# Kernel tuning notes

Hardware: AMD Instinct MI355X
Metric: run time of the kernel (lower is better)

## Reference

```python
import jax, jax.numpy as jnp
import numpy as np

B, L, D, H, DH, DL, NB = 8, 1024, 512, 8, 64, 64, 128
EPS = 1e-6


def layer_norm(x, g, b):
    m = jnp.mean(x, axis=-1, keepdims=True)
    v = jnp.mean((x - m) ** 2, axis=-1, keepdims=True)
    return (x - m) * jax.lax.rsqrt(v + EPS) * g + b


def rel_bias(timestamps, pos_w, ts_w):
    # position part: skew trick, pos_w has length 2L-1
    t = jnp.concatenate([pos_w, jnp.zeros((L,), pos_w.dtype)])  # (3L-1,)
    t = jnp.tile(t, L)[:-L].reshape(L, 3 * L - 2)
    rel_pos = t[:, L - 1:2 * L - 1]  # (L, L)
    # timestamp part: bucketized pairwise diffs of extended timestamps
    ext = jnp.concatenate([timestamps, timestamps[:, L - 1:L]], axis=1)  # (B, L+1)
    d = ext[:, 1:, None] - ext[:, None, :-1]  # (B, L, L)
    mag = jnp.maximum(jnp.abs(d).astype(jnp.float32), 1.0)
    bucket = jnp.clip((jnp.log(mag) / 0.301).astype(jnp.int32), 0, NB)
    rel_ts = ts_w[bucket]  # (B, L, L)
    return rel_pos[None] + rel_ts


def setup_inputs() -> dict:
    key = jax.random.key(0)
    ks = jax.random.split(key, 8)
    x = jax.random.normal(ks[0], (B, L, D), dtype=jnp.float32)
    timestamps = jnp.sort(jax.random.randint(ks[1], (B, L), 0, 1000000, dtype=jnp.int64), axis=1)
    attn_mask = jnp.triu(jnp.ones((L, L), jnp.float32), k=1)[None, None]  # 1 = masked (future)
    total_out = 2 * DL * H + 2 * DH * H
    uvqk_w = jax.random.normal(ks[2], (D, total_out), dtype=jnp.float32) * 0.02
    out_w = jax.random.normal(ks[3], (DL * H, D), dtype=jnp.float32) * 0.02
    out_b = jnp.zeros((D,), jnp.float32)
    ln1_g = jnp.ones((D,), jnp.float32); ln1_b = jnp.zeros((D,), jnp.float32)
    ln2_g = jnp.ones((DL * H,), jnp.float32); ln2_b = jnp.zeros((DL * H,), jnp.float32)
    ts_weights = jax.random.normal(ks[4], (NB + 1,), dtype=jnp.float32) * 0.02
    pos_weights = jax.random.normal(ks[5], (2 * L - 1,), dtype=jnp.float32) * 0.02
    return {"x": x, "timestamps": timestamps, "attn_mask": attn_mask,
            "uvqk_w": uvqk_w, "out_w": out_w, "out_b": out_b,
            "ln1_g": ln1_g, "ln1_b": ln1_b, "ln2_g": ln2_g, "ln2_b": ln2_b,
            "ts_weights": ts_weights, "pos_weights": pos_weights}


def reference(x, timestamps, attn_mask, uvqk_w, out_w, out_b,
              ln1_g, ln1_b, ln2_g, ln2_b, ts_weights, pos_weights):
    z = layer_norm(x, ln1_g, ln1_b)
    z = jax.nn.silu(z @ uvqk_w)  # linear_activation == 'silu'
    u, v, q, k = jnp.split(z, [DL * H, 2 * DL * H, 2 * DL * H + DH * H], axis=-1)
    q = q.reshape(B, L, H, DH)
    k = k.reshape(B, L, H, DH)
    v = v.reshape(B, L, H, DL)
    scores = jnp.einsum('bmhd,bnhd->bhmn', q, k)
    scores = scores + rel_bias(timestamps, pos_weights, ts_weights)[:, None]
    scores = jax.nn.silu(scores) / L * (1.0 - attn_mask)
    z = jnp.einsum('bhmn,bnhd->bmhd', scores, v).reshape(B, L, H * DL)
    z = layer_norm(z, ln2_g, ln2_b) * u  # gated LN
    return z @ out_w + out_b + x
```

## Files before the change

### kernel.cpp

```cpp
#include <hip/hip_runtime.h>
#include <math.h>

constexpr int Bc = 8;
constexpr int Lc = 1024;
constexpr int Dc = 512;
constexpr int Hc = 8;
constexpr int DHc = 64;
constexpr int DLc = 64;
constexpr int NBc = 128;
constexpr int TOTAL_OUT = 2 * DLc * Hc + 2 * DHc * Hc;
constexpr int ROWS = Bc * Lc;

using f32x4 = __attribute__((ext_vector_type(4))) float;
using s16x8 = __attribute__((ext_vector_type(8))) short;

__device__ __forceinline__ float bf2f(ushort u) {
    union { unsigned int i; float f; } v; v.i = ((unsigned int)u) << 16; return v.f;
}
__device__ __forceinline__ ushort f2bf(float f) {
    union { float f; unsigned int i; } v; v.f = f;
    unsigned int r = v.i + 0x7fffu + ((v.i >> 16) & 1u);
    return (ushort)(r >> 16);
}
__device__ __forceinline__ float silu(float x) {
    float e = __expf(-x);
    return x * __builtin_amdgcn_rcpf(1.0f + e);
}

__global__ __launch_bounds__(256) void transpose_cast(const float* __restrict__ in,
                                                      ushort* __restrict__ out,
                                                      int R, int C) {
    __shared__ float tile[32][33];
    int bc = blockIdx.x * 32, br = blockIdx.y * 32;
    int tx = threadIdx.x & 31, ty = threadIdx.x >> 5;
    for (int i = ty; i < 32; i += 8) {
        int r = br + i, c = bc + tx;
        tile[i][tx] = (r < R && c < C) ? in[(size_t)r * C + c] : 0.f;
    }
    __syncthreads();
    for (int i = ty; i < 32; i += 8) {
        int c = bc + i, r = br + tx;
        if (c < C && r < R) out[(size_t)c * R + r] = f2bf(tile[tx][i]);
    }
}

__global__ __launch_bounds__(256) void ln1_kernel(const float* __restrict__ x,
                                                  const float* __restrict__ g,
                                                  const float* __restrict__ bta,
                                                  ushort* __restrict__ outp) {
    int wid = threadIdx.x >> 6, lane = threadIdx.x & 63;
    int row = blockIdx.x * 4 + wid;
    const float4* xr = (const float4*)(x + (size_t)row * Dc);
    float4 a = xr[lane * 2], c = xr[lane * 2 + 1];
    float xv[8] = {a.x, a.y, a.z, a.w, c.x, c.y, c.z, c.w};
    float s = 0.f, q = 0.f;
#pragma unroll
    for (int i = 0; i < 8; i++) { s += xv[i]; q += xv[i] * xv[i]; }
#pragma unroll
    for (int off = 32; off; off >>= 1) { s += __shfl_xor(s, off); q += __shfl_xor(q, off); }
    float mean = s * (1.f / 512.f);
    float var  = q * (1.f / 512.f) - mean * mean;
    float rstd = rsqrtf(var + 1e-6f);
    const float4* gv = (const float4*)g; const float4* bv = (const float4*)bta;
    float4 g0 = gv[lane * 2], g1 = gv[lane * 2 + 1];
    float4 b0 = bv[lane * 2], b1 = bv[lane * 2 + 1];
    float G[8] = {g0.x, g0.y, g0.z, g0.w, g1.x, g1.y, g1.z, g1.w};
    float Bv[8] = {b0.x, b0.y, b0.z, b0.w, b1.x, b1.y, b1.z, b1.w};
    union { ushort u16[8]; uint4 v; } pk;
#pragma unroll
    for (int i = 0; i < 8; i++) pk.u16[i] = f2bf((xv[i] - mean) * rstd * G[i] + Bv[i]);
    ((uint4*)(outp + (size_t)row * Dc))[lane] = pk.v;
}

__global__ __launch_bounds__(256) void gemm1_kernel(const ushort* __restrict__ A,
                                                    const ushort* __restrict__ Bt,
                                                    ushort* __restrict__ Ub,
                                                    ushort* __restrict__ Vb,
                                                    ushort* __restrict__ Qb,
                                                    ushort* __restrict__ Kb) {
    __shared__ __align__(16) ushort As[128][72];
    __shared__ __align__(16) ushort Bs[128][72];
    int tid = threadIdx.x;
    int m0 = blockIdx.x * 128, n0 = blockIdx.y * 128;
    int w = tid >> 6, lane = tid & 63;
    int wm = (w >> 1) * 64, wn = (w & 1) * 64;
    f32x4 acc[4][4] = {};
    for (int k0 = 0; k0 < Dc; k0 += 64) {
        __syncthreads();
#pragma unroll
        for (int c = tid; c < 1024; c += 256) {
            int r = c >> 3, c8 = c & 7;
            *(uint4*)&As[r][c8 * 8] = *(const uint4*)&A[(size_t)(m0 + r) * Dc + k0 + c8 * 8];
            *(uint4*)&Bs[r][c8 * 8] = *(const uint4*)&Bt[(size_t)(n0 + r) * Dc + k0 + c8 * 8];
        }
        __syncthreads();
#pragma unroll
        for (int ks = 0; ks < 2; ++ks) {
            int kb = ks * 32 + (lane >> 4) * 8;
            s16x8 af[4], bfr[4];
#pragma unroll
            for (int i = 0; i < 4; i++) af[i] = *(const s16x8*)&As[wm + i * 16 + (lane & 15)][kb];
#pragma unroll
            for (int j = 0; j < 4; j++) bfr[j] = *(const s16x8*)&Bs[wn + j * 16 + (lane & 15)][kb];
#pragma unroll
            for (int i = 0; i < 4; i++)
#pragma unroll
                for (int j = 0; j < 4; j++)
                    acc[i][j] = __builtin_amdgcn_mfma_f32_16x16x32_bf16(af[i], bfr[j], acc[i][j], 0, 0, 0);
        }
    }
    int lr = (lane >> 4) * 4, lc = lane & 15;
#pragma unroll
    for (int i = 0; i < 4; i++)
#pragma unroll
        for (int j = 0; j < 4; j++) {
            int col = n0 + wn + j * 16 + lc;
            int sect = col >> 9, cc = col & 511;
            ushort* dst = (sect == 0) ? Ub : (sect == 1) ? Vb : (sect == 2) ? Qb : Kb;
#pragma unroll
            for (int r = 0; r < 4; r++) {
                int row = m0 + wm + i * 16 + lr + r;
                dst[(size_t)row * 512 + cc] = f2bf(silu(acc[i][j][r]));
            }
        }
}

__global__ __launch_bounds__(256) void attn_kernel(const ushort* __restrict__ Qb,
                                                   const ushort* __restrict__ Kb,
                                                   const ushort* __restrict__ Vb,
                                                   const int* __restrict__ ts,
                                                   const float* __restrict__ pos_w,
                                                   const float* __restrict__ ts_w,
                                                   ushort* __restrict__ Ob) {
    int mt = (gridDim.x - 1) - blockIdx.x;
    int h = blockIdx.y, b = blockIdx.z;
    __shared__ __align__(16) ushort Ks[64][72];
    __shared__ __align__(16) ushort VTs[64][72];
    __shared__ __align__(16) ushort Ps[128][72];
    __shared__ float tsw[NBc + 1];
    __shared__ float posw[2 * Lc - 1];
    int tid = threadIdx.x, w = tid >> 6, lane = tid & 63;
    const size_t hbase = ((size_t)b * Lc) * 512 + h * 64;
    const int m0 = mt * 128;
    for (int i2 = tid; i2 < 2 * Lc - 1; i2 += 256) posw[i2] = pos_w[i2];
    if (tid < NBc + 1) tsw[tid] = ts_w[tid];
    s16x8 qf[2][2];
#pragma unroll
    for (int i = 0; i < 2; i++)
#pragma unroll
        for (int ks = 0; ks < 2; ++ks) {
            int kb = ks * 32 + (lane >> 4) * 8;
            qf[i][ks] = *(const s16x8*)&Qb[hbase + (size_t)(m0 + w * 32 + i * 16 + (lane & 15)) * 512 + kb];
        }
    const int* tsb = ts + b * Lc;
    f32x4 acc_o[2][4] = {};
    int lr = (lane >> 4) * 4, lc = lane & 15;
    int ntiles = 2 * mt + 2;
    for (int nt = 0; nt < ntiles; ++nt) {
        int n0 = nt * 64;
        __syncthreads();
#pragma unroll
        for (int c = tid; c < 512; c += 256) {
            int r = c >> 3, c8 = c & 7;
            *(uint4*)&Ks[r][c8 * 8] = *(const uint4*)&Kb[hbase + (size_t)(n0 + r) * 512 + c8 * 8];
            uint4 vv = *(const uint4*)&Vb[hbase + (size_t)(n0 + r) * 512 + c8 * 8];
            ushort* pv = (ushort*)&vv;
#pragma unroll
            for (int e = 0; e < 8; e++) VTs[c8 * 8 + e][r] = pv[e];
        }
        __syncthreads();
        f32x4 s[2][4] = {};
#pragma unroll
        for (int ks = 0; ks < 2; ++ks) {
            int kb = ks * 32 + (lane >> 4) * 8;
            s16x8 bfr[4];
#pragma unroll
            for (int j = 0; j < 4; j++) bfr[j] = *(const s16x8*)&Ks[j * 16 + (lane & 15)][kb];
#pragma unroll
            for (int i = 0; i < 2; i++)
#pragma unroll
                for (int j = 0; j < 4; j++)
                    s[i][j] = __builtin_amdgcn_mfma_f32_16x16x32_bf16(qf[i][ks], bfr[j], s[i][j], 0, 0, 0);
        }
#pragma unroll
        for (int i = 0; i < 2; i++) {
            int mbase = m0 + w * 32 + i * 16 + lr;
            int me_r[4];
#pragma unroll
            for (int r = 0; r < 4; r++) {
                int mp = mbase + r + 1;
                me_r[r] = tsb[mp < Lc ? mp : (Lc - 1)];
            }
#pragma unroll
            for (int j = 0; j < 4; j++) {
                int ncol = n0 + j * 16 + lc;
                int tn = tsb[ncol];
#pragma unroll
                for (int r = 0; r < 4; r++) {
                    int m = mbase + r;
                    float val = 0.f;
                    if (ncol <= m) {
                        float mag = fmaxf(fabsf((float)(me_r[r] - tn)), 1.f);
                        int bkt = (int)(__log2f(mag) * 2.3028147f);
                        bkt = bkt < 0 ? 0 : (bkt > NBc ? NBc : bkt);
                        float sv = s[i][j][r] + posw[(Lc - 1) + ncol - m] + tsw[bkt];
                        val = silu(sv) * (1.f / (float)Lc);
                    }
                    Ps[w * 32 + i * 16 + lr + r][j * 16 + lc] = f2bf(val);
                }
            }
        }
#pragma unroll
        for (int ks = 0; ks < 2; ++ks) {
            int kb = ks * 32 + (lane >> 4) * 8;
            s16x8 pa[2], vb[4];
#pragma unroll
            for (int i = 0; i < 2; i++) pa[i] = *(const s16x8*)&Ps[w * 32 + i * 16 + (lane & 15)][kb];
#pragma unroll
            for (int j = 0; j < 4; j++) vb[j] = *(const s16x8*)&VTs[j * 16 + (lane & 15)][kb];
#pragma unroll
            for (int i = 0; i < 2; i++)
#pragma unroll
                for (int j = 0; j < 4; j++)
                    acc_o[i][j] = __builtin_amdgcn_mfma_f32_16x16x32_bf16(pa[i], vb[j], acc_o[i][j], 0, 0, 0);
        }
    }
#pragma unroll
    for (int i = 0; i < 2; i++)
#pragma unroll
        for (int j = 0; j < 4; j++)
#pragma unroll
            for (int r = 0; r < 4; r++) {
                int m = m0 + w * 32 + i * 16 + lr + r;
                Ob[hbase + (size_t)m * 512 + j * 16 + lc] = f2bf(acc_o[i][j][r]);
            }
}

__global__ __launch_bounds__(256) void ln2_kernel(const ushort* __restrict__ z,
                                                  const ushort* __restrict__ u,
                                                  const float* __restrict__ g,
                                                  const float* __restrict__ bta,
                                                  ushort* __restrict__ outp) {
    int wid = threadIdx.x >> 6, lane = threadIdx.x & 63;
    int row = blockIdx.x * 4 + wid;
    uint4 zv = ((const uint4*)(z + (size_t)row * 512))[lane];
    ushort* zu = (ushort*)&zv;
    float xv[8], s = 0.f, q = 0.f;
#pragma unroll
    for (int i = 0; i < 8; i++) { xv[i] = bf2f(zu[i]); s += xv[i]; q += xv[i] * xv[i]; }
#pragma unroll
    for (int off = 32; off; off >>= 1) { s += __shfl_xor(s, off); q += __shfl_xor(q, off); }
    float mean = s * (1.f / 512.f);
    float var  = q * (1.f / 512.f) - mean * mean;
    float rstd = rsqrtf(var + 1e-6f);
    uint4 uv = ((const uint4*)(u + (size_t)row * 512))[lane];
    ushort* uu = (ushort*)&uv;
    const float4* gv = (const float4*)g; const float4* bv = (const float4*)bta;
    float4 g0 = gv[lane * 2], g1 = gv[lane * 2 + 1];
    float4 b0 = bv[lane * 2], b1 = bv[lane * 2 + 1];
    float G[8] = {g0.x, g0.y, g0.z, g0.w, g1.x, g1.y, g1.z, g1.w};
    float Bv[8] = {b0.x, b0.y, b0.z, b0.w, b1.x, b1.y, b1.z, b1.w};
    union { ushort u16[8]; uint4 v; } pk;
#pragma unroll
    for (int i = 0; i < 8; i++)
        pk.u16[i] = f2bf(((xv[i] - mean) * rstd * G[i] + Bv[i]) * bf2f(uu[i]));
    ((uint4*)(outp + (size_t)row * 512))[lane] = pk.v;
}

__global__ __launch_bounds__(256) void gemm2_kernel(const ushort* __restrict__ A,
                                                    const ushort* __restrict__ Bt,
                                                    const float* __restrict__ ob,
                                                    const float* __restrict__ x,
                                                    float* __restrict__ outp) {
    __shared__ __align__(16) ushort As[128][72];
    __shared__ __align__(16) ushort Bs[128][72];
    int tid = threadIdx.x;
    int m0 = blockIdx.x * 128, n0 = blockIdx.y * 128;
    int w = tid >> 6, lane = tid & 63;
    int wm = (w >> 1) * 64, wn = (w & 1) * 64;
    f32x4 acc[4][4] = {};
    for (int k0 = 0; k0 < Dc; k0 += 64) {
        __syncthreads();
#pragma unroll
        for (int c = tid; c < 1024; c += 256) {
            int r = c >> 3, c8 = c & 7;
            *(uint4*)&As[r][c8 * 8] = *(const uint4*)&A[(size_t)(m0 + r) * Dc + k0 + c8 * 8];
            *(uint4*)&Bs[r][c8 * 8] = *(const uint4*)&Bt[(size_t)(n0 + r) * Dc + k0 + c8 * 8];
        }
        __syncthreads();
#pragma unroll
        for (int ks = 0; ks < 2; ++ks) {
            int kb = ks * 32 + (lane >> 4) * 8;
            s16x8 af[4], bfr[4];
#pragma unroll
            for (int i = 0; i < 4; i++) af[i] = *(const s16x8*)&As[wm + i * 16 + (lane & 15)][kb];
#pragma unroll
            for (int j = 0; j < 4; j++) bfr[j] = *(const s16x8*)&Bs[wn + j * 16 + (lane & 15)][kb];
#pragma unroll
            for (int i = 0; i < 4; i++)
#pragma unroll
                for (int j = 0; j < 4; j++)
                    acc[i][j] = __builtin_amdgcn_mfma_f32_16x16x32_bf16(af[i], bfr[j], acc[i][j], 0, 0, 0);
        }
    }
    int lr = (lane >> 4) * 4, lc = lane & 15;
#pragma unroll
    for (int i = 0; i < 4; i++)
#pragma unroll
        for (int j = 0; j < 4; j++) {
            int col = n0 + wn + j * 16 + lc;
            float bias = ob[col];
#pragma unroll
            for (int r = 0; r < 4; r++) {
                int row = m0 + wm + i * 16 + lr + r;
                size_t off = (size_t)row * 512 + col;
                outp[off] = acc[i][j][r] + bias + x[off];
            }
        }
}

extern "C" void kernel_launch(void* const* d_in, const int* in_sizes, int n_in,
                              void* d_out, int out_size, void* d_ws, size_t ws_size,
                              hipStream_t stream) {
    const float* x      = (const float*)d_in[0];
    const int*   tsp    = (const int*)d_in[1];
    const float* uvqk_w = (const float*)d_in[3];
    const float* out_w  = (const float*)d_in[4];
    const float* out_b  = (const float*)d_in[5];
    const float* ln1_g  = (const float*)d_in[6];
    const float* ln1_b  = (const float*)d_in[7];
    const float* ln2_g  = (const float*)d_in[8];
    const float* ln2_b  = (const float*)d_in[9];
    const float* ts_w   = (const float*)d_in[10];
    const float* pos_w  = (const float*)d_in[11];
    float* outp = (float*)d_out;

    char* ws = (char*)d_ws;
    size_t off = 0;
    auto alloc = [&](size_t bytes) { char* p = ws + off; off += (bytes + 255) & ~(size_t)255; return p; };
    const size_t MAT = (size_t)ROWS * 512 * sizeof(ushort);
    ushort* W1T = (ushort*)alloc((size_t)TOTAL_OUT * Dc * 2);
    ushort* W2T = (ushort*)alloc((size_t)Dc * Dc * 2);
    ushort* X1  = (ushort*)alloc(MAT);
    ushort* Ub  = (ushort*)alloc(MAT);
    ushort* Vb  = (ushort*)alloc(MAT);
    ushort* Qb  = (ushort*)alloc(MAT);
    ushort* Kb  = (ushort*)alloc(MAT);
    ushort* Ob  = (ushort*)alloc(MAT);
    ushort* A2  = X1;

    transpose_cast<<<dim3(TOTAL_OUT / 32, Dc / 32), 256, 0, stream>>>(uvqk_w, W1T, Dc, TOTAL_OUT);
    transpose_cast<<<dim3(Dc / 32, Dc / 32), 256, 0, stream>>>(out_w, W2T, Dc, Dc);
    ln1_kernel<<<ROWS / 4, 256, 0, stream>>>(x, ln1_g, ln1_b, X1);
    gemm1_kernel<<<dim3(ROWS / 128, TOTAL_OUT / 128), 256, 0, stream>>>(X1, W1T, Ub, Vb, Qb, Kb);
    attn_kernel<<<dim3(Lc / 128, Hc, Bc), 256, 0, stream>>>(Qb, Kb, Vb, tsp, pos_w, ts_w, Ob);
    ln2_kernel<<<ROWS / 4, 256, 0, stream>>>(Ob, Ub, ln2_g, ln2_b, A2);
    gemm2_kernel<<<dim3(ROWS / 128, Dc / 128), 256, 0, stream>>>(A2, W2T, out_b, x, outp);
}
```

Baseline: 263.6 us.

## Write V transposed from GEMM1 and read K/V fragments directly in attention

GEMM1 now writes V in a per-(batch, head) transposed layout, so attention no longer needs to transpose V through shared memory. The attention kernel drops K/V shared-memory staging and its block-wide barriers, loading MFMA fragments straight from global memory. It also shrinks the query tile to 64 rows, caches timestamps in LDS, and interleaves heavy and light causal tiles across block indices for load balance. In exchange, K/V tiles are re-read from global or L2 by every wave without shared reuse, and the transposed V stores from GEMM1 are less coalesced.

```diff
diff --git a/kernel.cpp b/kernel.cpp
--- a/kernel.cpp
+++ b/kernel.cpp
@@ -75,7 +75,7 @@
 __global__ __launch_bounds__(256) void gemm1_kernel(const ushort* __restrict__ A,
                                                     const ushort* __restrict__ Bt,
                                                     ushort* __restrict__ Ub,
-                                                    ushort* __restrict__ Vb,
+                                                    ushort* __restrict__ VTg,
                                                     ushort* __restrict__ Qb,
                                                     ushort* __restrict__ Kb) {
     __shared__ __align__(16) ushort As[128][72];
@@ -116,124 +116,114 @@
         for (int j = 0; j < 4; j++) {
             int col = n0 + wn + j * 16 + lc;
             int sect = col >> 9, cc = col & 511;
-            ushort* dst = (sect == 0) ? Ub : (sect == 1) ? Vb : (sect == 2) ? Qb : Kb;
-#pragma unroll
-            for (int r = 0; r < 4; r++) {
-                int row = m0 + wm + i * 16 + lr + r;
-                dst[(size_t)row * 512 + cc] = f2bf(silu(acc[i][j][r]));
+            int row0 = m0 + wm + i * 16 + lr;
+            if (sect == 1) {
+                int hh = cc >> 6, dd = cc & 63;
+                int bb = row0 >> 10, nn = row0 & 1023;
+                ushort4 pk;
+                pk.x = f2bf(silu(acc[i][j][0]));
+                pk.y = f2bf(silu(acc[i][j][1]));
+                pk.z = f2bf(silu(acc[i][j][2]));
+                pk.w = f2bf(silu(acc[i][j][3]));
+                *(ushort4*)&VTg[((size_t)((bb * 8 + hh) * 64 + dd)) * 1024 + nn] = pk;
+            } else {
+                ushort* dst = (sect == 0) ? Ub : (sect == 2) ? Qb : Kb;
+#pragma unroll
+                for (int r = 0; r < 4; r++)
+                    dst[(size_t)(row0 + r) * 512 + cc] = f2bf(silu(acc[i][j][r]));
             }
         }
 }
 
 __global__ __launch_bounds__(256) void attn_kernel(const ushort* __restrict__ Qb,
                                                    const ushort* __restrict__ Kb,
-                                                   const ushort* __restrict__ Vb,
+                                                   const ushort* __restrict__ VTg,
                                                    const int* __restrict__ ts,
                                                    const float* __restrict__ pos_w,
                                                    const float* __restrict__ ts_w,
                                                    ushort* __restrict__ Ob) {
-    int mt = (gridDim.x - 1) - blockIdx.x;
+    int bx = blockIdx.x;
+    int mt = (bx & 1) ? (bx >> 1) : (15 - (bx >> 1));
     int h = blockIdx.y, b = blockIdx.z;
-    __shared__ __align__(16) ushort Ks[64][72];
-    __shared__ __align__(16) ushort VTs[64][72];
-    __shared__ __align__(16) ushort Ps[128][72];
+    __shared__ __align__(16) ushort Ps[4][16][72];
+    __shared__ float posw[2 * Lc - 1];
     __shared__ float tsw[NBc + 1];
-    __shared__ float posw[2 * Lc - 1];
+    __shared__ int tss[Lc];
     int tid = threadIdx.x, w = tid >> 6, lane = tid & 63;
-    const size_t hbase = ((size_t)b * Lc) * 512 + h * 64;
-    const int m0 = mt * 128;
-    for (int i2 = tid; i2 < 2 * Lc - 1; i2 += 256) posw[i2] = pos_w[i2];
+    const size_t qkbase = ((size_t)b * Lc) * 512 + h * 64;
+    const size_t vtbase = ((size_t)((b * 8 + h) * 64)) * 1024;
+    const int m0 = mt * 64;
+    for (int i = tid; i < 2 * Lc - 1; i += 256) posw[i] = pos_w[i];
+    for (int i = tid; i < Lc; i += 256) tss[i] = ts[b * Lc + i];
     if (tid < NBc + 1) tsw[tid] = ts_w[tid];
-    s16x8 qf[2][2];
-#pragma unroll
-    for (int i = 0; i < 2; i++)
+    __syncthreads();
+
+    int lr = (lane >> 4) * 4, lc = lane & 15;
+    int kb0 = (lane >> 4) * 8;
+    s16x8 qf[2];
+#pragma unroll
+    for (int ks = 0; ks < 2; ++ks)
+        qf[ks] = *(const s16x8*)&Qb[qkbase + (size_t)(m0 + w * 16 + lc) * 512 + ks * 32 + kb0];
+    int mbase = m0 + w * 16 + lr;
+    int me_r[4];
+#pragma unroll
+    for (int r = 0; r < 4; r++) {
+        int mp = mbase + r + 1;
+        me_r[r] = tss[mp < Lc ? mp : (Lc - 1)];
+    }
+    f32x4 acc_o[4] = {};
+    for (int nt = 0; nt <= mt; ++nt) {
+        int n0 = nt * 64;
+        f32x4 s[4] = {};
 #pragma unroll
         for (int ks = 0; ks < 2; ++ks) {
-            int kb = ks * 32 + (lane >> 4) * 8;
-            qf[i][ks] = *(const s16x8*)&Qb[hbase + (size_t)(m0 + w * 32 + i * 16 + (lane & 15)) * 512 + kb];
-        }
-    const int* tsb = ts + b * Lc;
-    f32x4 acc_o[2][4] = {};
-    int lr = (lane >> 4) * 4, lc = lane & 15;
-    int ntiles = 2 * mt + 2;
-    for (int nt = 0; nt < ntiles; ++nt) {
-        int n0 = nt * 64;
-        __syncthreads();
-#pragma unroll
-        for (int c = tid; c < 512; c += 256) {
-            int r = c >> 3, c8 = c & 7;
-            *(uint4*)&Ks[r][c8 * 8] = *(const uint4*)&Kb[hbase + (size_t)(n0 + r) * 512 + c8 * 8];
-            uint4 vv = *(const uint4*)&Vb[hbase + (size_t)(n0 + r) * 512 + c8 * 8];
-            ushort* pv = (ushort*)&vv;
-#pragma unroll
-            for (int e = 0; e < 8; e++) VTs[c8 * 8 + e][r] = pv[e];
-        }
-        __syncthreads();
-        f32x4 s[2][4] = {};
+            int kb = ks * 32 + kb0;
+            s16x8 kf[4];
+#pragma unroll
+            for (int j = 0; j < 4; j++)
+                kf[j] = *(const s16x8*)&Kb[qkbase + (size_t)(n0 + j * 16 + lc) * 512 + kb];
+#pragma unroll
+            for (int j = 0; j < 4; j++)
+                s[j] = __builtin_amdgcn_mfma_f32_16x16x32_bf16(qf[ks], kf[j], s[j], 0, 0, 0);
+        }
+#pragma unroll
+        for (int j = 0; j < 4; j++) {
+            int ncol = n0 + j * 16 + lc;
+            int tn = tss[ncol];
+#pragma unroll
+            for (int r = 0; r < 4; r++) {
+                int m = mbase + r;
+                float val = 0.f;
+                if (ncol <= m) {
+                    float mag = fmaxf(fabsf((float)(me_r[r] - tn)), 1.f);
+                    int bkt = (int)(__log2f(mag) * 2.3028147f);
+                    bkt = bkt < 0 ? 0 : (bkt > NBc ? NBc : bkt);
+                    float sv = s[j][r] + posw[(Lc - 1) + ncol - m] + tsw[bkt];
+                    val = silu(sv) * (1.f / (float)Lc);
+                }
+                Ps[w][lr + r][j * 16 + lc] = f2bf(val);
+            }
+        }
 #pragma unroll
         for (int ks = 0; ks < 2; ++ks) {
-            int kb = ks * 32 + (lane >> 4) * 8;
-            s16x8 bfr[4];
-#pragma unroll
-            for (int j = 0; j < 4; j++) bfr[j] = *(const s16x8*)&Ks[j * 16 + (lane & 15)][kb];
-#pragma unroll
-            for (int i = 0; i < 2; i++)
-#pragma unroll
-                for (int j = 0; j < 4; j++)
-                    s[i][j] = __builtin_amdgcn_mfma_f32_16x16x32_bf16(qf[i][ks], bfr[j], s[i][j], 0, 0, 0);
-        }
-#pragma unroll
-        for (int i = 0; i < 2; i++) {
-            int mbase = m0 + w * 32 + i * 16 + lr;
-            int me_r[4];
-#pragma unroll
-            for (int r = 0; r < 4; r++) {
-                int mp = mbase + r + 1;
-                me_r[r] = tsb[mp < Lc ? mp : (Lc - 1)];
-            }
-#pragma unroll
-            for (int j = 0; j < 4; j++) {
-                int ncol = n0 + j * 16 + lc;
-                int tn = tsb[ncol];
-#pragma unroll
-                for (int r = 0; r < 4; r++) {
-                    int m = mbase + r;
-                    float val = 0.f;
-                    if (ncol <= m) {
-                        float mag = fmaxf(fabsf((float)(me_r[r] - tn)), 1.f);
-                        int bkt = (int)(__log2f(mag) * 2.3028147f);
-                        bkt = bkt < 0 ? 0 : (bkt > NBc ? NBc : bkt);
-                        float sv = s[i][j][r] + posw[(Lc - 1) + ncol - m] + tsw[bkt];
-                        val = silu(sv) * (1.f / (float)Lc);
-                    }
-                    Ps[w * 32 + i * 16 + lr + r][j * 16 + lc] = f2bf(val);
-                }
-            }
-        }
-#pragma unroll
-        for (int ks = 0; ks < 2; ++ks) {
-            int kb = ks * 32 + (lane >> 4) * 8;
-            s16x8 pa[2], vb[4];
-#pragma unroll
-            for (int i = 0; i < 2; i++) pa[i] = *(const s16x8*)&Ps[w * 32 + i * 16 + (lane & 15)][kb];
-#pragma unroll
-            for (int j = 0; j < 4; j++) vb[j] = *(const s16x8*)&VTs[j * 16 + (lane & 15)][kb];
-#pragma unroll
-            for (int i = 0; i < 2; i++)
-#pragma unroll
-                for (int j = 0; j < 4; j++)
-                    acc_o[i][j] = __builtin_amdgcn_mfma_f32_16x16x32_bf16(pa[i], vb[j], acc_o[i][j], 0, 0, 0);
-        }
-    }
-#pragma unroll
-    for (int i = 0; i < 2; i++)
-#pragma unroll
-        for (int j = 0; j < 4; j++)
-#pragma unroll
-            for (int r = 0; r < 4; r++) {
-                int m = m0 + w * 32 + i * 16 + lr + r;
-                Ob[hbase + (size_t)m * 512 + j * 16 + lc] = f2bf(acc_o[i][j][r]);
-            }
+            int kb = ks * 32 + kb0;
+            s16x8 pa = *(const s16x8*)&Ps[w][lc][kb];
+            s16x8 vb[4];
+#pragma unroll
+            for (int j = 0; j < 4; j++)
+                vb[j] = *(const s16x8*)&VTg[vtbase + (size_t)(j * 16 + lc) * 1024 + n0 + kb];
+#pragma unroll
+            for (int j = 0; j < 4; j++)
+                acc_o[j] = __builtin_amdgcn_mfma_f32_16x16x32_bf16(pa, vb[j], acc_o[j], 0, 0, 0);
+        }
+    }
+#pragma unroll
+    for (int j = 0; j < 4; j++)
+#pragma unroll
+        for (int r = 0; r < 4; r++) {
+            int m = mbase + r;
+            Ob[qkbase + (size_t)m * 512 + j * 16 + lc] = f2bf(acc_o[j][r]);
+        }
 }
 
 __global__ __launch_bounds__(256) void ln2_kernel(const ushort* __restrict__ z,
@@ -343,7 +333,7 @@
     ushort* W2T = (ushort*)alloc((size_t)Dc * Dc * 2);
     ushort* X1  = (ushort*)alloc(MAT);
     ushort* Ub  = (ushort*)alloc(MAT);
-    ushort* Vb  = (ushort*)alloc(MAT);
+    ushort* VTg = (ushort*)alloc(MAT);
     ushort* Qb  = (ushort*)alloc(MAT);
     ushort* Kb  = (ushort*)alloc(MAT);
     ushort* Ob  = (ushort*)alloc(MAT);
@@ -352,8 +342,8 @@
     transpose_cast<<<dim3(TOTAL_OUT / 32, Dc / 32), 256, 0, stream>>>(uvqk_w, W1T, Dc, TOTAL_OUT);
     transpose_cast<<<dim3(Dc / 32, Dc / 32), 256, 0, stream>>>(out_w, W2T, Dc, Dc);
     ln1_kernel<<<ROWS / 4, 256, 0, stream>>>(x, ln1_g, ln1_b, X1);
-    gemm1_kernel<<<dim3(ROWS / 128, TOTAL_OUT / 128), 256, 0, stream>>>(X1, W1T, Ub, Vb, Qb, Kb);
-    attn_kernel<<<dim3(Lc / 128, Hc, Bc), 256, 0, stream>>>(Qb, Kb, Vb, tsp, pos_w, ts_w, Ob);
+    gemm1_kernel<<<dim3(ROWS / 128, TOTAL_OUT / 128), 256, 0, stream>>>(X1, W1T, Ub, VTg, Qb, Kb);
+    attn_kernel<<<dim3(16, Hc, Bc), 256, 0, stream>>>(Qb, Kb, VTg, tsp, pos_w, ts_w, Ob);
     ln2_kernel<<<ROWS / 4, 256, 0, stream>>>(Ob, Ub, ln2_g, ln2_b, A2);
     gemm2_kernel<<<dim3(ROWS / 128, Dc / 128), 256, 0, stream>>>(A2, W2T, out_b, x, outp);
 }
```

New measurement: 284.1 us. 1.08x slower.
